# Optimization experiments

Measured on AMD Instinct MI355X. Metric: run time of the kernel, lower is better.

Reference implementation:

```python
import jax, jax.numpy as jnp
import numpy as np

# Per-task block sizes, sorted descending (powers of 2), as in _InverseLogDetCache
N = (262144, 65536, 16384)
TOTAL = 262144 + 65536 + 16384  # 344064
DIAG_SHIFT = 10.0  # keeps Schur complement S away from 0 (plays role of noise)


def setup_inputs() -> dict:
    key = jax.random.key(0)
    ks = jax.random.split(key, 14)
    rn = lambda k, n: jax.random.normal(k, (n,), dtype=jnp.float32)
    return {
        "lam00_re": rn(ks[0], N[0]) + DIAG_SHIFT,
        "lam00_im": rn(ks[1], N[0]),
        "lam01_re": rn(ks[2], N[0]),
        "lam01_im": rn(ks[3], N[0]),
        "lam02_re": rn(ks[4], N[0]),
        "lam02_im": rn(ks[5], N[0]),
        "lam11_re": rn(ks[6], N[1]) + DIAG_SHIFT,
        "lam11_im": rn(ks[7], N[1]),
        "lam12_re": rn(ks[8], N[1]),
        "lam12_im": rn(ks[9], N[1]),
        "lam22_re": rn(ks[10], N[2]) + DIAG_SHIFT,
        "lam22_im": rn(ks[11], N[2]),
        "z_re": rn(ks[12], TOTAL),
        "z_im": rn(ks[13], TOTAL),
    }


def _step(A, B, lam_ll, n_l):
    """One recursive block Schur-complement update.
    A: (Ra, Ra, na) complex current inverse; B: (Ra*r, n_l) off-diag lam block;
    lam_ll: (n_l,) diagonal lam; returns updated A (R+1, R+1, n_l) and logdet inc."""
    Ra, na = A.shape[0], A.shape[-1]
    r = na // n_l
    Bvec = B.reshape(Ra, -1)                              # (Ra, na)
    T = (Bvec[None, :, :] * A).sum(1).reshape(-1, n_l)    # (R, n_l), R = Ra*r
    M = (B.conj() * T).sum(0)                             # (n_l,)
    S = lam_ll - M                                        # Schur complement diag
    logdet_inc = jnp.log(jnp.abs(S)).sum()
    P = T / S                                             # (R, n_l)
    C = P[:, None, :] * T[None, :, :].conj()              # (R, R, n_l)
    # scatter-add old inverse A into the refined block structure of C
    ii0, ii1, ii2 = jnp.meshgrid(jnp.arange(Ra), jnp.arange(Ra), jnp.arange(na), indexing='ij')
    ii0, ii1, ii2 = ii0.ravel(), ii1.ravel(), ii2.ravel()
    jj0 = ii2 % n_l
    jj1 = ii2 // n_l
    C = C.at[ii0 * r + jj1, ii1 * r + jj1, jj0].add(A.reshape(-1))
    ur = jnp.concatenate([C, -P[:, None, :]], axis=1)                       # (R, R+1, n_l)
    br = jnp.concatenate([-P.conj()[None, :, :], (1.0 / S)[None, None, :]], axis=1)  # (1, R+1, n_l)
    return jnp.concatenate([ur, br], axis=0), logdet_inc


def _forward(lams, z):
    A = (1.0 / lams[(0, 0)])[None, None, :]               # (1, 1, N[0])
    logdet = jnp.log(jnp.abs(lams[(0, 0)])).sum()
    for l in range(1, len(N)):
        B = jnp.concatenate([lams[(k, l)] for k in range(l)], axis=0).reshape(-1, N[l])
        A, inc = _step(A, B, lams[(l, l)], N[l])
        logdet = logdet + inc
    # tilde-to-tilde gram matrix solve: z (TOTAL,) -> (1, R, n_min) * A, sum block rows
    n_min = N[-1]
    zb = z.reshape(1, -1, n_min)                          # (1, 21, n_min)
    zout = (zb * A).sum(-2).reshape(-1)                   # (TOTAL,)
    return A, logdet, zout


def reference(lam00_re, lam00_im, lam01_re, lam01_im, lam02_re, lam02_im,
              lam11_re, lam11_im, lam12_re, lam12_im, lam22_re, lam22_im,
              z_re, z_im):
    lams = {
        (0, 0): lam00_re + 1j * lam00_im,
        (0, 1): lam01_re + 1j * lam01_im,
        (0, 2): lam02_re + 1j * lam02_im,
        (1, 1): lam11_re + 1j * lam11_im,
        (1, 2): lam12_re + 1j * lam12_im,
        (2, 2): lam22_re + 1j * lam22_im,
    }
    z = z_re + 1j * z_im
    A, logdet, zout = _forward(lams, z)
    return (jnp.stack([A.real, A.imag]), logdet, jnp.stack([zout.real, zout.imag]))
```

## Files before the change

### kernel.cpp

```cpp
#include <hip/hip_runtime.h>

#define N2 16384
#define N1 65536
#define N0 262144

#define WS_T2_RE   0
#define WS_T2_IM   (20*N2)
#define WS_M2P_RE  (40*N2)
#define WS_M2P_IM  (44*N2)
#define WS_P1_RE   (48*N2)
#define WS_P1_IM   (64*N2)
#define WS_T1_RE   (80*N2)
#define WS_T1_IM   (96*N2)
#define WS_I00_RE  (112*N2)
#define WS_I00_IM  (128*N2)
#define WS_IS1_RE  (144*N2)
#define WS_IS1_IM  (148*N2)
#define WS_LD_BYTE ((size_t)(152*N2)*4)

#define OUT_AIM 7225344
#define OUT_LD  14450688
#define OUT_ZRE 14450689
#define OUT_ZIM 14794753

__device__ __forceinline__ void block_reduce_atomic(float v, double* acc,
                                                    float* wsum) {
#pragma unroll
    for (int off = 32; off > 0; off >>= 1) v += __shfl_down(v, off, 64);
    const int lane = threadIdx.x & 63;
    const int wid  = threadIdx.x >> 6;
    if (lane == 0) wsum[wid] = v;
    __syncthreads();
    if (threadIdx.x == 0)
        atomicAdd(acc, (double)(wsum[0] + wsum[1] + wsum[2] + wsum[3]));
}

__global__ __launch_bounds__(256) void stage12_kernel(
    const float* __restrict__ l00r, const float* __restrict__ l00i,
    const float* __restrict__ l01r, const float* __restrict__ l01i,
    const float* __restrict__ l02r, const float* __restrict__ l02i,
    const float* __restrict__ l11r, const float* __restrict__ l11i,
    const float* __restrict__ l12r, const float* __restrict__ l12i,
    float* __restrict__ ws, double* __restrict__ ld_acc)
{
    const int m = blockIdx.x * 256 + threadIdx.x;
    const int u = m >> 14;
    const int j = m & (N2 - 1);

    float ld = 0.f;
    float i0r[4], i0i[4], t1r[4], t1i[4], p1r[4], p1i[4];
    float m1r = 0.f, m1i = 0.f;
#pragma unroll
    for (int k = 0; k < 4; ++k) {
        const int i = k * N1 + m;
        const float ar = l00r[i], ai = l00i[i];
        const float br = l01r[i], bi = l01i[i];
        const float d  = ar*ar + ai*ai;
        const float rd = 1.f / d;
        ld += 0.5f * logf(d);
        const float xr = ar * rd, xi = -ai * rd;
        i0r[k] = xr; i0i[k] = xi;
        const float tr = br*xr - bi*xi;
        const float ti = br*xi + bi*xr;
        t1r[k] = tr; t1i[k] = ti;
        m1r += br*tr + bi*ti;
        m1i += br*ti - bi*tr;
    }
    const float s1r = l11r[m] - m1r;
    const float s1i = l11i[m] - m1i;
    const float ds1 = s1r*s1r + s1i*s1i;
    ld += 0.5f * logf(ds1);
    const float rds1 = 1.f / ds1;
    const float is1r = s1r * rds1, is1i = -s1i * rds1;
#pragma unroll
    for (int k = 0; k < 4; ++k) {
        p1r[k] = t1r[k]*is1r - t1i[k]*is1i;
        p1i[k] = t1r[k]*is1i + t1i[k]*is1r;
    }

    float bcr[5], bci[5];
#pragma unroll
    for (int a = 0; a < 4; ++a) { bcr[a] = l02r[a*N1+m]; bci[a] = l02i[a*N1+m]; }
    bcr[4] = l12r[m]; bci[4] = l12i[m];

    float wr = -bcr[4], wi = -bci[4];
#pragma unroll
    for (int b = 0; b < 4; ++b) {
        wr += bcr[b]*t1r[b] + bci[b]*t1i[b];
        wi += bci[b]*t1r[b] - bcr[b]*t1i[b];
    }
    float t2r[5], t2i[5];
#pragma unroll
    for (int a = 0; a < 4; ++a) {
        t2r[a] = p1r[a]*wr - p1i[a]*wi + bcr[a]*i0r[a] - bci[a]*i0i[a];
        t2i[a] = p1r[a]*wi + p1i[a]*wr + bcr[a]*i0i[a] + bci[a]*i0r[a];
    }
    {
        float vr = bcr[4]*is1r - bci[4]*is1i;
        float vi = bcr[4]*is1i + bci[4]*is1r;
#pragma unroll
        for (int b = 0; b < 4; ++b) {
            vr -= bcr[b]*p1r[b] + bci[b]*p1i[b];
            vi -= bci[b]*p1r[b] - bcr[b]*p1i[b];
        }
        t2r[4] = vr; t2i[4] = vi;
    }

    float m2r = 0.f, m2i = 0.f;
#pragma unroll
    for (int a = 0; a < 5; ++a) {
        const int q = a*4 + u;
        ws[WS_T2_RE + q*N2 + j] = t2r[a];
        ws[WS_T2_IM + q*N2 + j] = t2i[a];
        m2r += bcr[a]*t2r[a] + bci[a]*t2i[a];
        m2i += bcr[a]*t2i[a] - bci[a]*t2r[a];
    }
    ws[WS_M2P_RE + u*N2 + j] = m2r;
    ws[WS_M2P_IM + u*N2 + j] = m2i;
#pragma unroll
    for (int k = 0; k < 4; ++k) {
        ws[WS_P1_RE  + k*N1 + m] = p1r[k];
        ws[WS_P1_IM  + k*N1 + m] = p1i[k];
        ws[WS_T1_RE  + k*N1 + m] = t1r[k];
        ws[WS_T1_IM  + k*N1 + m] = t1i[k];
        ws[WS_I00_RE + k*N1 + m] = i0r[k];
        ws[WS_I00_IM + k*N1 + m] = i0i[k];
    }
    ws[WS_IS1_RE + m] = is1r;
    ws[WS_IS1_IM + m] = is1i;

    __shared__ float wsum[4];
    block_reduce_atomic(ld, ld_acc, wsum);
}

__global__ __launch_bounds__(256) void stage3_kernel(
    const float* __restrict__ l22r, const float* __restrict__ l22i,
    const float* __restrict__ zre, const float* __restrict__ zim,
    const float* __restrict__ ws, float* __restrict__ out,
    double* __restrict__ ld_acc)
{
    const int j = blockIdx.x * 256 + threadIdx.x;
    const int p = blockIdx.y;

    float s2r = l22r[j], s2i = l22i[j];
#pragma unroll
    for (int u = 0; u < 4; ++u) {
        s2r -= ws[WS_M2P_RE + u*N2 + j];
        s2i -= ws[WS_M2P_IM + u*N2 + j];
    }
    const float ds2  = s2r*s2r + s2i*s2i;
    const float rds2 = 1.f / ds2;
    const float is2r = s2r * rds2, is2i = -s2i * rds2;

    float zar = 0.f, zai = 0.f;
    if (p == 20) {
#pragma unroll
        for (int q = 0; q < 21; ++q) {
            float ar, ai;
            if (q < 20) {
                const float tr = ws[WS_T2_RE + q*N2 + j];
                const float ti = ws[WS_T2_IM + q*N2 + j];
                const float pr = tr*is2r - ti*is2i;
                const float pi = tr*is2i + ti*is2r;
                ar = -pr; ai = pi;
            } else { ar = is2r; ai = is2i; }
            out[(p*21 + q)*N2 + j]           = ar;
            out[OUT_AIM + (p*21 + q)*N2 + j] = ai;
            const float zqr = zre[q*N2 + j], zqi = zim[q*N2 + j];
            zar += zqr*ar - zqi*ai;
            zai += zqr*ai + zqi*ar;
        }
    } else {
        const int a  = p >> 2;
        const int u  = p & 3;
        const int mu = u*N2 + j;
        const float tpr = ws[WS_T2_RE + p*N2 + j];
        const float tpi = ws[WS_T2_IM + p*N2 + j];
        const float ppr = tpr*is2r - tpi*is2i;
        const float ppi = tpr*is2i + tpi*is2r;
        float par=0.f, pai=0.f, ir=0.f, ii=0.f, js1r=0.f, js1i=0.f;
        float t1br[4], t1bi[4], p1br[4], p1bi[4];
        if (a < 4) {
            par = ws[WS_P1_RE  + a*N1 + mu]; pai = ws[WS_P1_IM  + a*N1 + mu];
            ir  = ws[WS_I00_RE + a*N1 + mu]; ii  = ws[WS_I00_IM + a*N1 + mu];
#pragma unroll
            for (int b = 0; b < 4; ++b) {
                t1br[b] = ws[WS_T1_RE + b*N1 + mu];
                t1bi[b] = ws[WS_T1_IM + b*N1 + mu];
            }
        } else {
#pragma unroll
            for (int b = 0; b < 4; ++b) {
                p1br[b] = ws[WS_P1_RE + b*N1 + mu];
                p1bi[b] = ws[WS_P1_IM + b*N1 + mu];
            }
            js1r = ws[WS_IS1_RE + mu]; js1i = ws[WS_IS1_IM + mu];
        }
#pragma unroll
        for (int q = 0; q < 21; ++q) {
            float ar, ai;
            if (q < 20) {
                const float tr = ws[WS_T2_RE + q*N2 + j];
                const float ti = ws[WS_T2_IM + q*N2 + j];
                ar = ppr*tr + ppi*ti;
                ai = ppi*tr - ppr*ti;
                if ((q & 3) == u) {
                    const int b = q >> 2;
                    if (a < 4) {
                        if (b < 4) {
                            ar += par*t1br[b] + pai*t1bi[b];
                            ai += pai*t1br[b] - par*t1bi[b];
                            if (b == a) { ar += ir; ai += ii; }
                        } else { ar -= par; ai -= pai; }
                    } else {
                        if (b < 4) { ar -= p1br[b]; ai += p1bi[b]; }
                        else       { ar += js1r; ai += js1i; }
                    }
                }
            } else { ar = -ppr; ai = -ppi; }
            out[(p*21 + q)*N2 + j]           = ar;
            out[OUT_AIM + (p*21 + q)*N2 + j] = ai;
            const float zqr = zre[q*N2 + j], zqi = zim[q*N2 + j];
            zar += zqr*ar - zqi*ai;
            zai += zqr*ai + zqi*ar;
        }
    }
    out[OUT_ZRE + p*N2 + j] = zar;
    out[OUT_ZIM + p*N2 + j] = zai;

    if (p == 0) {
        __shared__ float wsum[4];
        block_reduce_atomic(0.5f * logf(ds2), ld_acc, wsum);
    }
}

__global__ void finalize_kernel(const double* __restrict__ acc,
                                float* __restrict__ out) {
    out[OUT_LD] = (float)(*acc);
}

extern "C" void kernel_launch(void* const* d_in, const int* in_sizes, int n_in,
                              void* d_out, int out_size, void* d_ws, size_t ws_size,
                              hipStream_t stream)
{
    const float* l00r = (const float*)d_in[0];
    const float* l00i = (const float*)d_in[1];
    const float* l01r = (const float*)d_in[2];
    const float* l01i = (const float*)d_in[3];
    const float* l02r = (const float*)d_in[4];
    const float* l02i = (const float*)d_in[5];
    const float* l11r = (const float*)d_in[6];
    const float* l11i = (const float*)d_in[7];
    const float* l12r = (const float*)d_in[8];
    const float* l12i = (const float*)d_in[9];
    const float* l22r = (const float*)d_in[10];
    const float* l22i = (const float*)d_in[11];
    const float* zre  = (const float*)d_in[12];
    const float* zim  = (const float*)d_in[13];
    float*  out    = (float*)d_out;
    float*  ws     = (float*)d_ws;
    double* ld_acc = (double*)((char*)d_ws + WS_LD_BYTE);

    hipMemsetAsync(ld_acc, 0, sizeof(double), stream);
    stage12_kernel<<<dim3(N1/256), dim3(256), 0, stream>>>(
        l00r,l00i,l01r,l01i,l02r,l02i,l11r,l11i,l12r,l12i, ws, ld_acc);
    stage3_kernel<<<dim3(N2/256, 21), dim3(256), 0, stream>>>(
        l22r,l22i,zre,zim, ws, out, ld_acc);
    finalize_kernel<<<1, 1, 0, stream>>>(ld_acc, out);
}
```

Before: 129.9 us.

## Fuse stage12 into stage3 with per-block recompute and deterministic logdet partials

Merges the two main kernels into one: each of the 21 blocks per column recomputes the stage-1/2 quantities for all four sub-indices in registers instead of reading them back from a workspace. This drops the workspace writes and reads, the memset and the atomic double accumulation; logdet now goes through per-block partials summed by a single-warp finalize kernel. The price is redoing the stage-1/2 input loads and arithmetic (including the log and divide calls) 21 times and holding more registers per thread, which may lower occupancy.

```diff
diff --git a/kernel.cpp b/kernel.cpp
--- a/kernel.cpp
+++ b/kernel.cpp
@@ -3,154 +3,116 @@
 #define N2 16384
 #define N1 65536
 #define N0 262144
-
-#define WS_T2_RE   0
-#define WS_T2_IM   (20*N2)
-#define WS_M2P_RE  (40*N2)
-#define WS_M2P_IM  (44*N2)
-#define WS_P1_RE   (48*N2)
-#define WS_P1_IM   (64*N2)
-#define WS_T1_RE   (80*N2)
-#define WS_T1_IM   (96*N2)
-#define WS_I00_RE  (112*N2)
-#define WS_I00_IM  (128*N2)
-#define WS_IS1_RE  (144*N2)
-#define WS_IS1_IM  (148*N2)
-#define WS_LD_BYTE ((size_t)(152*N2)*4)
 
 #define OUT_AIM 7225344
 #define OUT_LD  14450688
 #define OUT_ZRE 14450689
 #define OUT_ZIM 14794753
 
-__device__ __forceinline__ void block_reduce_atomic(float v, double* acc,
-                                                    float* wsum) {
-#pragma unroll
-    for (int off = 32; off > 0; off >>= 1) v += __shfl_down(v, off, 64);
-    const int lane = threadIdx.x & 63;
-    const int wid  = threadIdx.x >> 6;
-    if (lane == 0) wsum[wid] = v;
-    __syncthreads();
-    if (threadIdx.x == 0)
-        atomicAdd(acc, (double)(wsum[0] + wsum[1] + wsum[2] + wsum[3]));
-}
-
-__global__ __launch_bounds__(256) void stage12_kernel(
+__global__ __launch_bounds__(256) void fused_kernel(
     const float* __restrict__ l00r, const float* __restrict__ l00i,
     const float* __restrict__ l01r, const float* __restrict__ l01i,
     const float* __restrict__ l02r, const float* __restrict__ l02i,
     const float* __restrict__ l11r, const float* __restrict__ l11i,
     const float* __restrict__ l12r, const float* __restrict__ l12i,
-    float* __restrict__ ws, double* __restrict__ ld_acc)
+    const float* __restrict__ l22r, const float* __restrict__ l22i,
+    const float* __restrict__ zre,  const float* __restrict__ zim,
+    float* __restrict__ out, double* __restrict__ ld_partial)
 {
-    const int m = blockIdx.x * 256 + threadIdx.x;
-    const int u = m >> 14;
-    const int j = m & (N2 - 1);
-
+    const int j   = blockIdx.x * 256 + threadIdx.x;
+    const int p   = blockIdx.y;
+    const int a_p = p >> 2, u_p = p & 3;
+
+    float t2r[20], t2i[20];
+    float m2tr = 0.f, m2ti = 0.f;
     float ld = 0.f;
-    float i0r[4], i0i[4], t1r[4], t1i[4], p1r[4], p1i[4];
-    float m1r = 0.f, m1i = 0.f;
-#pragma unroll
-    for (int k = 0; k < 4; ++k) {
-        const int i = k * N1 + m;
-        const float ar = l00r[i], ai = l00i[i];
-        const float br = l01r[i], bi = l01i[i];
-        const float d  = ar*ar + ai*ai;
-        const float rd = 1.f / d;
-        ld += 0.5f * logf(d);
-        const float xr = ar * rd, xi = -ai * rd;
-        i0r[k] = xr; i0i[k] = xi;
-        const float tr = br*xr - bi*xi;
-        const float ti = br*xi + bi*xr;
-        t1r[k] = tr; t1i[k] = ti;
-        m1r += br*tr + bi*ti;
-        m1i += br*ti - bi*tr;
+    float st1r[4], st1i[4], sp1r[4], sp1i[4];
+    float si0r = 0.f, si0i = 0.f, ss1r = 0.f, ss1i = 0.f;
+
+#pragma unroll
+    for (int u = 0; u < 4; ++u) {
+        const int m = u * N2 + j;
+        float i0r[4], i0i[4], t1r[4], t1i[4], p1r[4], p1i[4];
+        float m1r = 0.f, m1i = 0.f;
+#pragma unroll
+        for (int k = 0; k < 4; ++k) {
+            const int i = k * N1 + m;
+            const float ar = l00r[i], ai = l00i[i];
+            const float br = l01r[i], bi = l01i[i];
+            const float d  = ar*ar + ai*ai;
+            const float rd = 1.f / d;
+            ld += 0.5f * logf(d);
+            const float xr = ar * rd, xi = -ai * rd;
+            i0r[k] = xr; i0i[k] = xi;
+            const float tr = br*xr - bi*xi;
+            const float ti = br*xi + bi*xr;
+            t1r[k] = tr; t1i[k] = ti;
+            m1r += br*tr + bi*ti;
+            m1i += br*ti - bi*tr;
+        }
+        const float s1r = l11r[m] - m1r;
+        const float s1i = l11i[m] - m1i;
+        const float ds1 = s1r*s1r + s1i*s1i;
+        ld += 0.5f * logf(ds1);
+        const float rds1 = 1.f / ds1;
+        const float is1r = s1r * rds1, is1i = -s1i * rds1;
+#pragma unroll
+        for (int k = 0; k < 4; ++k) {
+            p1r[k] = t1r[k]*is1r - t1i[k]*is1i;
+            p1i[k] = t1r[k]*is1i + t1i[k]*is1r;
+        }
+
+        float bcr[5], bci[5];
+#pragma unroll
+        for (int a = 0; a < 4; ++a) { bcr[a] = l02r[a*N1+m]; bci[a] = l02i[a*N1+m]; }
+        bcr[4] = l12r[m]; bci[4] = l12i[m];
+
+        float wr = -bcr[4], wi = -bci[4];
+#pragma unroll
+        for (int b = 0; b < 4; ++b) {
+            wr += bcr[b]*t1r[b] + bci[b]*t1i[b];
+            wi += bci[b]*t1r[b] - bcr[b]*t1i[b];
+        }
+        float ur[5], ui[5];
+#pragma unroll
+        for (int a = 0; a < 4; ++a) {
+            ur[a] = p1r[a]*wr - p1i[a]*wi + bcr[a]*i0r[a] - bci[a]*i0i[a];
+            ui[a] = p1r[a]*wi + p1i[a]*wr + bcr[a]*i0i[a] + bci[a]*i0r[a];
+        }
+        {
+            float vr = bcr[4]*is1r - bci[4]*is1i;
+            float vi = bcr[4]*is1i + bci[4]*is1r;
+#pragma unroll
+            for (int b = 0; b < 4; ++b) {
+                vr -= bcr[b]*p1r[b] + bci[b]*p1i[b];
+                vi -= bci[b]*p1r[b] - bcr[b]*p1i[b];
+            }
+            ur[4] = vr; ui[4] = vi;
+        }
+#pragma unroll
+        for (int a = 0; a < 5; ++a) {
+            t2r[a*4 + u] = ur[a];
+            t2i[a*4 + u] = ui[a];
+            m2tr += bcr[a]*ur[a] + bci[a]*ui[a];
+            m2ti += bcr[a]*ui[a] - bci[a]*ur[a];
+        }
+        if (u == u_p) {
+#pragma unroll
+            for (int b = 0; b < 4; ++b) {
+                st1r[b] = t1r[b]; st1i[b] = t1i[b];
+                sp1r[b] = p1r[b]; sp1i[b] = p1i[b];
+            }
+            si0r = i0r[a_p & 3]; si0i = i0i[a_p & 3];
+            ss1r = is1r;         ss1i = is1i;
+        }
     }
-    const float s1r = l11r[m] - m1r;
-    const float s1i = l11i[m] - m1i;
-    const float ds1 = s1r*s1r + s1i*s1i;
-    ld += 0.5f * logf(ds1);
-    const float rds1 = 1.f / ds1;
-    const float is1r = s1r * rds1, is1i = -s1i * rds1;
-#pragma unroll
-    for (int k = 0; k < 4; ++k) {
-        p1r[k] = t1r[k]*is1r - t1i[k]*is1i;
-        p1i[k] = t1r[k]*is1i + t1i[k]*is1r;
-    }
-
-    float bcr[5], bci[5];
-#pragma unroll
-    for (int a = 0; a < 4; ++a) { bcr[a] = l02r[a*N1+m]; bci[a] = l02i[a*N1+m]; }
-    bcr[4] = l12r[m]; bci[4] = l12i[m];
-
-    float wr = -bcr[4], wi = -bci[4];
-#pragma unroll
-    for (int b = 0; b < 4; ++b) {
-        wr += bcr[b]*t1r[b] + bci[b]*t1i[b];
-        wi += bci[b]*t1r[b] - bcr[b]*t1i[b];
-    }
-    float t2r[5], t2i[5];
-#pragma unroll
-    for (int a = 0; a < 4; ++a) {
-        t2r[a] = p1r[a]*wr - p1i[a]*wi + bcr[a]*i0r[a] - bci[a]*i0i[a];
-        t2i[a] = p1r[a]*wi + p1i[a]*wr + bcr[a]*i0i[a] + bci[a]*i0r[a];
-    }
-    {
-        float vr = bcr[4]*is1r - bci[4]*is1i;
-        float vi = bcr[4]*is1i + bci[4]*is1r;
-#pragma unroll
-        for (int b = 0; b < 4; ++b) {
-            vr -= bcr[b]*p1r[b] + bci[b]*p1i[b];
-            vi -= bci[b]*p1r[b] - bcr[b]*p1i[b];
-        }
-        t2r[4] = vr; t2i[4] = vi;
-    }
-
-    float m2r = 0.f, m2i = 0.f;
-#pragma unroll
-    for (int a = 0; a < 5; ++a) {
-        const int q = a*4 + u;
-        ws[WS_T2_RE + q*N2 + j] = t2r[a];
-        ws[WS_T2_IM + q*N2 + j] = t2i[a];
-        m2r += bcr[a]*t2r[a] + bci[a]*t2i[a];
-        m2i += bcr[a]*t2i[a] - bci[a]*t2r[a];
-    }
-    ws[WS_M2P_RE + u*N2 + j] = m2r;
-    ws[WS_M2P_IM + u*N2 + j] = m2i;
-#pragma unroll
-    for (int k = 0; k < 4; ++k) {
-        ws[WS_P1_RE  + k*N1 + m] = p1r[k];
-        ws[WS_P1_IM  + k*N1 + m] = p1i[k];
-        ws[WS_T1_RE  + k*N1 + m] = t1r[k];
-        ws[WS_T1_IM  + k*N1 + m] = t1i[k];
-        ws[WS_I00_RE + k*N1 + m] = i0r[k];
-        ws[WS_I00_IM + k*N1 + m] = i0i[k];
-    }
-    ws[WS_IS1_RE + m] = is1r;
-    ws[WS_IS1_IM + m] = is1i;
-
-    __shared__ float wsum[4];
-    block_reduce_atomic(ld, ld_acc, wsum);
-}
-
-__global__ __launch_bounds__(256) void stage3_kernel(
-    const float* __restrict__ l22r, const float* __restrict__ l22i,
-    const float* __restrict__ zre, const float* __restrict__ zim,
-    const float* __restrict__ ws, float* __restrict__ out,
-    double* __restrict__ ld_acc)
-{
-    const int j = blockIdx.x * 256 + threadIdx.x;
-    const int p = blockIdx.y;
-
-    float s2r = l22r[j], s2i = l22i[j];
-#pragma unroll
-    for (int u = 0; u < 4; ++u) {
-        s2r -= ws[WS_M2P_RE + u*N2 + j];
-        s2i -= ws[WS_M2P_IM + u*N2 + j];
-    }
+
+    const float s2r = l22r[j] - m2tr;
+    const float s2i = l22i[j] - m2ti;
     const float ds2  = s2r*s2r + s2i*s2i;
     const float rds2 = 1.f / ds2;
     const float is2r = s2r * rds2, is2i = -s2i * rds2;
+    ld += 0.5f * logf(ds2);
 
     float zar = 0.f, zai = 0.f;
     if (p == 20) {
@@ -158,10 +120,8 @@
         for (int q = 0; q < 21; ++q) {
             float ar, ai;
             if (q < 20) {
-                const float tr = ws[WS_T2_RE + q*N2 + j];
-                const float ti = ws[WS_T2_IM + q*N2 + j];
-                const float pr = tr*is2r - ti*is2i;
-                const float pi = tr*is2i + ti*is2r;
+                const float pr = t2r[q]*is2r - t2i[q]*is2i;
+                const float pi = t2r[q]*is2i + t2i[q]*is2r;
                 ar = -pr; ai = pi;
             } else { ar = is2r; ai = is2i; }
             out[(p*21 + q)*N2 + j]           = ar;
@@ -171,50 +131,25 @@
             zai += zqr*ai + zqi*ar;
         }
     } else {
-        const int a  = p >> 2;
-        const int u  = p & 3;
-        const int mu = u*N2 + j;
-        const float tpr = ws[WS_T2_RE + p*N2 + j];
-        const float tpi = ws[WS_T2_IM + p*N2 + j];
-        const float ppr = tpr*is2r - tpi*is2i;
-        const float ppi = tpr*is2i + tpi*is2r;
-        float par=0.f, pai=0.f, ir=0.f, ii=0.f, js1r=0.f, js1i=0.f;
-        float t1br[4], t1bi[4], p1br[4], p1bi[4];
-        if (a < 4) {
-            par = ws[WS_P1_RE  + a*N1 + mu]; pai = ws[WS_P1_IM  + a*N1 + mu];
-            ir  = ws[WS_I00_RE + a*N1 + mu]; ii  = ws[WS_I00_IM + a*N1 + mu];
-#pragma unroll
-            for (int b = 0; b < 4; ++b) {
-                t1br[b] = ws[WS_T1_RE + b*N1 + mu];
-                t1bi[b] = ws[WS_T1_IM + b*N1 + mu];
-            }
-        } else {
-#pragma unroll
-            for (int b = 0; b < 4; ++b) {
-                p1br[b] = ws[WS_P1_RE + b*N1 + mu];
-                p1bi[b] = ws[WS_P1_IM + b*N1 + mu];
-            }
-            js1r = ws[WS_IS1_RE + mu]; js1i = ws[WS_IS1_IM + mu];
-        }
+        const float ppr = t2r[p]*is2r - t2i[p]*is2i;
+        const float ppi = t2r[p]*is2i + t2i[p]*is2r;
 #pragma unroll
         for (int q = 0; q < 21; ++q) {
             float ar, ai;
             if (q < 20) {
-                const float tr = ws[WS_T2_RE + q*N2 + j];
-                const float ti = ws[WS_T2_IM + q*N2 + j];
-                ar = ppr*tr + ppi*ti;
-                ai = ppi*tr - ppr*ti;
-                if ((q & 3) == u) {
+                ar = ppr*t2r[q] + ppi*t2i[q];
+                ai = ppi*t2r[q] - ppr*t2i[q];
+                if ((q & 3) == u_p) {
                     const int b = q >> 2;
-                    if (a < 4) {
+                    if (a_p < 4) {
                         if (b < 4) {
-                            ar += par*t1br[b] + pai*t1bi[b];
-                            ai += pai*t1br[b] - par*t1bi[b];
-                            if (b == a) { ar += ir; ai += ii; }
-                        } else { ar -= par; ai -= pai; }
+                            ar += sp1r[a_p]*st1r[b] + sp1i[a_p]*st1i[b];
+                            ai += sp1i[a_p]*st1r[b] - sp1r[a_p]*st1i[b];
+                            if (b == a_p) { ar += si0r; ai += si0i; }
+                        } else { ar -= sp1r[a_p]; ai -= sp1i[a_p]; }
                     } else {
-                        if (b < 4) { ar -= p1br[b]; ai += p1bi[b]; }
-                        else       { ar += js1r; ai += js1i; }
+                        if (b < 4) { ar -= sp1r[b]; ai += sp1i[b]; }
+                        else       { ar += ss1r; ai += ss1i; }
                     }
                 }
             } else { ar = -ppr; ai = -ppi; }
@@ -229,14 +164,26 @@
     out[OUT_ZIM + p*N2 + j] = zai;
 
     if (p == 0) {
+        float v = ld;
+#pragma unroll
+        for (int off = 32; off > 0; off >>= 1) v += __shfl_down(v, off, 64);
         __shared__ float wsum[4];
-        block_reduce_atomic(0.5f * logf(ds2), ld_acc, wsum);
+        const int lane = threadIdx.x & 63;
+        const int wid  = threadIdx.x >> 6;
+        if (lane == 0) wsum[wid] = v;
+        __syncthreads();
+        if (threadIdx.x == 0)
+            ld_partial[blockIdx.x] =
+                (double)wsum[0] + (double)wsum[1] + (double)wsum[2] + (double)wsum[3];
     }
 }
 
-__global__ void finalize_kernel(const double* __restrict__ acc,
+__global__ void finalize_kernel(const double* __restrict__ part,
                                 float* __restrict__ out) {
-    out[OUT_LD] = (float)(*acc);
+    double v = part[threadIdx.x];
+#pragma unroll
+    for (int off = 32; off > 0; off >>= 1) v += __shfl_down(v, off, 64);
+    if (threadIdx.x == 0) out[OUT_LD] = (float)v;
 }
 
 extern "C" void kernel_launch(void* const* d_in, const int* in_sizes, int n_in,
@@ -257,14 +204,11 @@
     const float* l22i = (const float*)d_in[11];
     const float* zre  = (const float*)d_in[12];
     const float* zim  = (const float*)d_in[13];
-    float*  out    = (float*)d_out;
-    float*  ws     = (float*)d_ws;
-    double* ld_acc = (double*)((char*)d_ws + WS_LD_BYTE);
-
-    hipMemsetAsync(ld_acc, 0, sizeof(double), stream);
-    stage12_kernel<<<dim3(N1/256), dim3(256), 0, stream>>>(
-        l00r,l00i,l01r,l01i,l02r,l02i,l11r,l11i,l12r,l12i, ws, ld_acc);
-    stage3_kernel<<<dim3(N2/256, 21), dim3(256), 0, stream>>>(
-        l22r,l22i,zre,zim, ws, out, ld_acc);
-    finalize_kernel<<<1, 1, 0, stream>>>(ld_acc, out);
+    float*  out        = (float*)d_out;
+    double* ld_partial = (double*)d_ws;
+
+    fused_kernel<<<dim3(N2/256, 21), dim3(256), 0, stream>>>(
+        l00r,l00i,l01r,l01i,l02r,l02i,l11r,l11i,l12r,l12i,l22r,l22i,
+        zre,zim, out, ld_partial);
+    finalize_kernel<<<1, 64, 0, stream>>>(ld_partial, out);
 }
```

Measured after the change: 136.5 us. +5.1%, slower.
